# Kernel tuning notes

Hardware: AMD Instinct MI355X
Metric: run time of the kernel (lower is better)

Reference implementation:

```python
import jax, jax.numpy as jnp
import numpy as np

BS = 256          # batch size
N = 1000          # n_step_per_batch
ORDER = 2         # derivative order -> 3 vars (u, u', u'') per step
D = ORDER + 1
STEP_LOGIT = float(np.log(0.001 / 0.999))  # logit(0.001); sigmoid -> 0.001 step size


def mlp(x, w1, b1, w2, b2, w3, b3):
    h = jax.nn.relu(x @ w1 + b1)
    h = jax.nn.relu(h @ w2 + b2)
    return h @ w3 + b3


def build_A(c, h):
    # c: (N, 3) per-step equation coefficients; h: (N-1,) step sizes.
    # Rows: [1 initial-value] + [N equation] + [2*(N-1) Taylor smoothness (d=0,1)].
    R = 1 + N + 2 * (N - 1)
    i = jnp.arange(N)
    j = jnp.arange(N - 1)
    ones = jnp.ones(N - 1, c.dtype)
    rows = jnp.concatenate([
        jnp.array([0]),
        jnp.repeat(1 + i, 3),
        jnp.repeat(1 + N + 2 * j, 4),
        jnp.repeat(2 + N + 2 * j, 3)])
    cols = jnp.concatenate([
        jnp.array([0]),
        (i[:, None] * 3 + jnp.arange(3)).ravel(),
        jnp.stack([3 * j, 3 * j + 1, 3 * j + 2, 3 * (j + 1)], axis=1).ravel(),
        jnp.stack([3 * j + 1, 3 * j + 2, 3 * j + 4], axis=1).ravel()])
    vals = jnp.concatenate([
        jnp.ones(1, c.dtype),
        c.ravel(),
        jnp.stack([-ones, -h, -h * h / 2, ones], axis=1).ravel(),
        jnp.stack([-ones, -h, ones], axis=1).ravel()])
    return jnp.zeros((R, 3 * N), c.dtype).at[rows, cols].add(vals)


def ode_solve(coeffs, rhs, init_iv, steps):
    # coeffs (bs,1,N,3), rhs (bs,N,1), init_iv (bs,1), steps (bs,1,N-1)
    # coeffs/steps are batch-uniform in this model -> single shared system matrix.
    c = coeffs[0, 0]
    h = steps[0, 0]
    A = build_A(c, h)                       # (R, 3N)
    R = A.shape[0]
    b = jnp.zeros((R, BS), A.dtype)
    b = b.at[0].set(init_iv[:, 0]).at[1:1 + N].set(rhs[:, :, 0].T)
    AtA = A.T @ A + 1e-8 * jnp.eye(3 * N, dtype=A.dtype)
    u = jnp.linalg.solve(AtA, A.T @ b)      # (3N, BS) least-squares trajectory
    resid = A @ u - b
    eps = jnp.sqrt(jnp.sum(resid * resid, axis=0))  # (BS,) equation slack norm
    u = u.reshape(N, 3, BS)
    x0 = u[:, 0].T[:, :, None]              # (bs, N, 1)
    x1 = u[:, 1].T[:, :, None]
    x2 = u[:, 2].T[:, :, None]
    return x0, x1, x2, eps, steps


def reference(pin, ptime, pw1, pb1, pw2, pb2, pw3, pb3,
              tw1, tb1, tw2, tb2, tw3, tb3,
              nw1, nb1, nw2, nb2, nw3, nb3, net_iv):
    xi = mlp(pin, pw1, pb1, pw2, pb2, pw3, pb3).reshape(1, 3)
    ts = mlp(ptime, tw1, tb1, tw2, tb2, tw3, tb3).reshape(1, N)
    xi = jnp.tile(xi, (BS, 1))
    ts = jnp.tile(ts, (BS, 1))
    alpha = xi[:, 0:1][:, None, :]                 # (bs,1,1)
    beta = xi[:, 1:2][:, None, :]
    powr = jax.nn.sigmoid(xi[:, 2:3][:, None, :])
    ts = ts[:, None, :]                            # (bs,1,N)
    var = mlp(net_iv.reshape(BS, -1), nw1, nb1, nw2, nb2, nw3, nb3).reshape(BS, 1, N)
    rhs = jnp.abs(alpha * ts + beta * ts ** 2) ** powr * var ** 2 + ts
    rhs = jnp.transpose(rhs, (0, 2, 1))            # (bs, N, 1)
    coeffs = jnp.broadcast_to(jnp.array([0.0, 1.0, 0.0], net_iv.dtype), (BS, 1, N, 3))
    init_iv = var[:, :, 0]                         # (bs, 1)
    steps = jax.nn.sigmoid(jnp.full((BS, 1, N - 1), STEP_LOGIT, net_iv.dtype))
    x0, x1, x2, eps, steps = ode_solve(coeffs, rhs, init_iv, steps)
    x0 = jnp.transpose(x0, (0, 2, 1))              # (bs, 1, N)
    var = jnp.transpose(var, (0, 2, 1))            # (bs, N, 1)
    return (x0, steps, eps, var, ts[:, 0, :], alpha, beta, powr)


def setup_inputs() -> dict:
    key = jax.random.key(0)
    ks = jax.random.split(key, 24)
    f32 = jnp.float32

    def w(k, shape, scale=0.03):
        return (scale * jax.random.normal(k, shape)).astype(f32)

    inp = {
        "pin": w(ks[0], (1, 64), 1.0),
        "ptime": w(ks[1], (1, 64), 1.0),
        "pw1": w(ks[2], (64, 1024)), "pb1": jnp.zeros((1024,), f32),
        "pw2": w(ks[3], (1024, 1024)), "pb2": jnp.zeros((1024,), f32),
        "pw3": w(ks[4], (1024, 3)), "pb3": jnp.zeros((3,), f32),
        "tw1": w(ks[5], (64, 1024)), "tb1": jnp.zeros((1024,), f32),
        "tw2": w(ks[6], (1024, 1024)), "tb2": jnp.zeros((1024,), f32),
        "tw3": w(ks[7], (1024, N)), "tb3": jnp.zeros((N,), f32),
        "nw1": w(ks[8], (N, 1024)), "nb1": jnp.zeros((1024,), f32),
        "nw2": w(ks[9], (1024, 1024)), "nb2": jnp.zeros((1024,), f32),
        "nw3": w(ks[10], (1024, N)), "nb3": jnp.zeros((N,), f32),
        "net_iv": jax.random.normal(ks[11], (BS, N)).astype(f32),
    }
    return inp
```

## Files before the change

### kernel.cpp

```cpp
#include <hip/hip_runtime.h>
#include <math.h>

#define NN 1000
#define NIT 4
#define NKT 16

typedef _Float16 f16;
typedef _Float16 f16x8 __attribute__((ext_vector_type(8)));
typedef _Float16 f16x2 __attribute__((ext_vector_type(2)));
typedef float    f32x4 __attribute__((ext_vector_type(4)));

#define WS_H1P 0
#define WS_H1T 1024
#define WS_H2P 2048
#define WS_H2T 3072
#define WS_TS  4096
#define WS_XI  5120
#define WF_H1  802816
#define WF_H2  1064960
#define WF_BT2 2375680
#define WF_BT3 3424256

#define O_X0    0
#define O_STEP  256000
#define O_EPS   511744
#define O_VAR   512000
#define O_TS    768000
#define O_ALPHA 1024000
#define O_BETA  1024256
#define O_POWR  1024512

__device__ __forceinline__ void conv_bt_body(int idx, const float* __restrict__ W, int K0, int NW,
                                             f16* __restrict__ BT, float (*T)[32][33])
{
    const int tid = threadIdx.x;
    const int tx = tid & 31, ty = tid >> 5;
    const int kt = (idx & 31) * 32, ntile = (idx >> 5) * 32;
    #pragma unroll
    for (int i = 0; i < 4; ++i) {
        int k = kt + ty + i * 8, n = ntile + tx;
        (*T)[ty + i * 8][tx] = (k < K0 && n < NW) ? W[(size_t)k * NW + n] : 0.f;
    }
    __syncthreads();
    #pragma unroll
    for (int i = 0; i < 4; ++i) {
        int n = ntile + ty + i * 8, k = kt + tx;
        BT[(size_t)n * 1024 + k] = (f16)(*T)[tx][ty + i * 8];
    }
}

__device__ __forceinline__ void l1_body(int sub, const float* __restrict__ pin,
    const float* __restrict__ pw1, const float* __restrict__ pb1,
    const float* __restrict__ ptime, const float* __restrict__ tw1, const float* __restrict__ tb1,
    float* __restrict__ ws, float* sin_)
{
    const int tid = threadIdx.x;
    const bool tp = sub >= 4;
    const float* in = tp ? ptime : pin;
    const float* W  = tp ? tw1 : pw1;
    const float* B  = tp ? tb1 : pb1;
    float* outp = ws + (tp ? WS_H1T : WS_H1P);
    const int bxl = sub & 3;
    if (tid < 64) sin_[tid] = in[tid];
    __syncthreads();
    const int u = bxl * 256 + tid;
    float acc = B[u];
    #pragma unroll 16
    for (int k = 0; k < 64; ++k) acc += sin_[k] * W[k * 1024 + u];
    outp[u] = fmaxf(acc, 0.f);
}

__device__ __forceinline__ void l2_body(int lb, const float* __restrict__ pw2, const float* __restrict__ pb2,
    const float* __restrict__ tw2, const float* __restrict__ tb2, float* __restrict__ ws,
    float (*red)[16][17])
{
    const bool tp = lb >= 64;
    const float* h = ws + (tp ? WS_H1T : WS_H1P);
    const float* W = tp ? tw2 : pw2;
    const float* B = tp ? tb2 : pb2;
    float* outp = ws + (tp ? WS_H2T : WS_H2P);
    const int u0 = (lb & 63) * 16;
    const int tid = threadIdx.x, ul = tid & 15, kc = tid >> 4;
    const float* wp = W + u0 + ul;
    float acc = 0.f;
    const int kbase = kc * 64;
    #pragma unroll 8
    for (int k = 0; k < 64; ++k) acc += h[kbase + k] * wp[(size_t)(kbase + k) * 1024];
    (*red)[kc][ul] = acc; __syncthreads();
    for (int s = 8; s; s >>= 1) { if (kc < s) (*red)[kc][ul] += (*red)[kc + s][ul]; __syncthreads(); }
    if (tid < 16) outp[u0 + tid] = fmaxf((*red)[0][tid] + B[u0 + tid], 0.f);
}

__device__ __forceinline__ void l3_body(int lb, const float* __restrict__ pw3, const float* __restrict__ pb3,
    const float* __restrict__ tw3, const float* __restrict__ tb3,
    float* __restrict__ ws, float* __restrict__ out,
    float (*red)[16][17], float* redx)
{
    const int tid = threadIdx.x;
    if (lb == 64) {
        const float* h2p = ws + WS_H2P;
        float p[3] = {0.f, 0.f, 0.f};
        for (int k = tid; k < 1024; k += 256) {
            float h = h2p[k];
            p[0] += h * pw3[k * 3 + 0];
            p[1] += h * pw3[k * 3 + 1];
            p[2] += h * pw3[k * 3 + 2];
        }
        float xi[3];
        #pragma unroll
        for (int j = 0; j < 3; ++j) {
            redx[tid] = p[j]; __syncthreads();
            for (int s = 128; s > 0; s >>= 1) {
                if (tid < s) redx[tid] += redx[tid + s];
                __syncthreads();
            }
            xi[j] = redx[0] + pb3[j];
            __syncthreads();
        }
        float alpha = xi[0], beta = xi[1];
        float powr = 1.f / (1.f + expf(-xi[2]));
        if (tid == 0) { ws[WS_XI + 0] = alpha; ws[WS_XI + 1] = beta; ws[WS_XI + 2] = powr; }
        out[O_ALPHA + tid] = alpha;
        out[O_BETA  + tid] = beta;
        out[O_POWR  + tid] = powr;
    } else {
        const float* h = ws + WS_H2T;
        const int u0 = lb * 16;
        const int ul = tid & 15, kc = tid >> 4;
        const int u = u0 + ul;
        float acc = 0.f;
        const int kbase = kc * 64;
        if (u < NN) {
            #pragma unroll 8
            for (int k = 0; k < 64; ++k) acc += h[kbase + k] * tw3[(size_t)(kbase + k) * NN + u];
        }
        (*red)[kc][ul] = acc; __syncthreads();
        for (int s = 8; s; s >>= 1) { if (kc < s) (*red)[kc][ul] += (*red)[kc + s][ul]; __syncthreads(); }
        if (tid < 16 && u0 + tid < NN) ws[WS_TS + u0 + tid] = (*red)[0][tid] + tb3[u0 + tid];
    }
}

__device__ __forceinline__ void gemm_conv_body(int bx,
    const float* __restrict__ Af, int ldA, int K0,
    const float* __restrict__ W, int NW, const float* __restrict__ bias,
    f16* __restrict__ Cf16,
    f16 (*As)[32][72], f16 (*Bs)[32][72])
{
    const int tid = threadIdx.x;
    const int lane = tid & 63, wave = tid >> 6;
    const int wm = wave >> 1, wn = wave & 1;
    const int m0 = (bx >> 5) * 32, n0b = (bx & 31) * 32;

    const int sarow = tid >> 3, sac = (tid & 7) * 8;
    const int sbk = (tid >> 3) * 2, sbn = (tid & 7) * 4;
    const int bcol_ok = (n0b + sbn) < NW;

    f16x8 pa; float4 pb0, pb1;

    auto loadA = [&](int k0, f16x8& o) {
        float4 x = {0.f,0.f,0.f,0.f}, y = {0.f,0.f,0.f,0.f};
        if (k0 + sac < K0) {
            const float* p = Af + (size_t)(m0 + sarow) * ldA + k0 + sac;
            x = *(const float4*)p;
            y = *(const float4*)(p + 4);
        }
        f16x8 h = {(f16)x.x,(f16)x.y,(f16)x.z,(f16)x.w,
                   (f16)y.x,(f16)y.y,(f16)y.z,(f16)y.w};
        o = h;
    };
    auto loadB = [&](int k0, float4& b0, float4& b1) {
        b0 = {0.f,0.f,0.f,0.f}; b1 = {0.f,0.f,0.f,0.f};
        const int r0 = k0 + sbk;
        if (bcol_ok) {
            const float* p = W + (size_t)r0 * NW + n0b + sbn;
            if (r0 < K0)     b0 = *(const float4*)p;
            if (r0 + 1 < K0) b1 = *(const float4*)(p + NW);
        }
    };
    auto storeA = [&](int buf, const f16x8& v) {
        *(f16x8*)&As[buf][sarow][sac] = v;
    };
    auto storeB = [&](int buf, const float4& b0, const float4& b1) {
        f16x2 v0 = {(f16)b0.x, (f16)b1.x}; *(f16x2*)&Bs[buf][sbn + 0][sbk] = v0;
        f16x2 v1 = {(f16)b0.y, (f16)b1.y}; *(f16x2*)&Bs[buf][sbn + 1][sbk] = v1;
        f16x2 v2 = {(f16)b0.z, (f16)b1.z}; *(f16x2*)&Bs[buf][sbn + 2][sbk] = v2;
        f16x2 v3 = {(f16)b0.w, (f16)b1.w}; *(f16x2*)&Bs[buf][sbn + 3][sbk] = v3;
    };

    f32x4 acc = {0.f, 0.f, 0.f, 0.f};

    loadA(0, pa); loadB(0, pb0, pb1);
    storeA(0, pa); storeB(0, pb0, pb1);
    loadA(64, pa); loadB(64, pb0, pb1);
    __syncthreads();

    const int arow = wm * 16 + (lane & 15);
    const int brow = wn * 16 + (lane & 15);
    const int kf = (lane >> 4) * 8;

    #pragma unroll 2
    for (int t = 0; t < NKT; ++t) {
        const int cur = t & 1;
        f16x8 na; float4 nb0 = {}, nb1 = {};
        if (t + 2 < NKT) { loadA((t + 2) * 64, na); loadB((t + 2) * 64, nb0, nb1); }

        const f16x8 a0 = *(const f16x8*)&As[cur][arow][kf];
        const f16x8 b0 = *(const f16x8*)&Bs[cur][brow][kf];
        acc = __builtin_amdgcn_mfma_f32_16x16x32_f16(a0, b0, acc, 0, 0, 0);
        const f16x8 a1 = *(const f16x8*)&As[cur][arow][32 + kf];
        const f16x8 b1 = *(const f16x8*)&Bs[cur][brow][32 + kf];
        acc = __builtin_amdgcn_mfma_f32_16x16x32_f16(a1, b1, acc, 0, 0, 0);

        __syncthreads();
        if (t + 1 < NKT) {
            storeA(cur ^ 1, pa);
            storeB(cur ^ 1, pb0, pb1);
        }
        pa = na; pb0 = nb0; pb1 = nb1;
        __syncthreads();
    }

    const int col = n0b + wn * 16 + (lane & 15);
    const int row = m0 + wm * 16 + (lane >> 4) * 4;
    const float bs = (col < NW) ? bias[col] : 0.f;
    #pragma unroll
    for (int j = 0; j < 4; ++j) {
        float v = fmaxf(acc[j] + bs, 0.f);
        Cf16[(size_t)(row + j) * 1024 + col] = (f16)v;
    }
}

template<bool F16OUT>
__device__ __forceinline__ void gemm16_body(int bx, const f16* __restrict__ A, const f16* __restrict__ BT,
    const float* __restrict__ bias, int NW, f16* __restrict__ Cf16, float* __restrict__ Cf32, int ldc,
    f16 (*As)[32][72], f16 (*Bs)[32][72])
{
    const int tid = threadIdx.x;
    const int lane = tid & 63, wave = tid >> 6;
    const int wm = wave >> 1, wn = wave & 1;
    const int m0 = (bx >> 5) * 32, n0 = (bx & 31) * 32;
    const int srow = tid >> 3, sc = tid & 7;
    const float4* gA = (const float4*)(A  + (size_t)(m0 + srow) * 1024 + sc * 8);
    const float4* gB = (const float4*)(BT + (size_t)(n0 + srow) * 1024 + sc * 8);

    f32x4 acc = {0.f, 0.f, 0.f, 0.f};

    float4 ra = gA[0], rb = gB[0];
    *(float4*)&As[0][srow][sc * 8] = ra;
    *(float4*)&Bs[0][srow][sc * 8] = rb;
    ra = gA[8]; rb = gB[8];
    __syncthreads();

    const int arow = wm * 16 + (lane & 15);
    const int brow = wn * 16 + (lane & 15);
    const int kf = (lane >> 4) * 8;

    #pragma unroll 2
    for (int t = 0; t < NKT; ++t) {
        const int cur = t & 1;
        float4 ra2 = {}, rb2 = {};
        if (t + 2 < NKT) { ra2 = gA[(t + 2) * 8]; rb2 = gB[(t + 2) * 8]; }

        const f16x8 a0 = *(const f16x8*)&As[cur][arow][kf];
        const f16x8 b0 = *(const f16x8*)&Bs[cur][brow][kf];
        acc = __builtin_amdgcn_mfma_f32_16x16x32_f16(a0, b0, acc, 0, 0, 0);
        const f16x8 a1 = *(const f16x8*)&As[cur][arow][32 + kf];
        const f16x8 b1 = *(const f16x8*)&Bs[cur][brow][32 + kf];
        acc = __builtin_amdgcn_mfma_f32_16x16x32_f16(a1, b1, acc, 0, 0, 0);

        __syncthreads();
        if (t + 1 < NKT) {
            *(float4*)&As[cur ^ 1][srow][sc * 8] = ra;
            *(float4*)&Bs[cur ^ 1][srow][sc * 8] = rb;
        }
        ra = ra2; rb = rb2;
        __syncthreads();
    }

    const int col = n0 + wn * 16 + (lane & 15);
    const int row = m0 + wm * 16 + (lane >> 4) * 4;
    const float bs = (col < NW) ? bias[col] : 0.f;
    #pragma unroll
    for (int j = 0; j < 4; ++j) {
        float v = acc[j] + bs;
        if (F16OUT) {
            v = fmaxf(v, 0.f);
            Cf16[(size_t)(row + j) * 1024 + col] = (f16)v;
        } else if (col < NW) {
            Cf32[(size_t)(row + j) * ldc + col] = v;
        }
    }
}

__global__ __launch_bounds__(256) void k_s1(const float* __restrict__ net_iv,
    const float* __restrict__ nw1, const float* __restrict__ nb1, const float* __restrict__ nw2,
    const float* __restrict__ pin, const float* __restrict__ pw1, const float* __restrict__ pb1,
    const float* __restrict__ ptime, const float* __restrict__ tw1, const float* __restrict__ tb1,
    float* __restrict__ ws, f16* __restrict__ wsh)
{
    __shared__ f16 As[2][32][72];
    __shared__ f16 Bs[2][32][72];
    __shared__ float T[32][33];
    __shared__ float sin_[64];
    const int bx = blockIdx.x;
    if (bx < 256) {
        gemm_conv_body(bx, net_iv, 1000, 1000, nw1, 1024, nb1, wsh + WF_H1, As, Bs);
    } else if (bx < 264) {
        l1_body(bx - 256, pin, pw1, pb1, ptime, tw1, tb1, ws, sin_);
    } else {
        conv_bt_body(bx - 264, nw2, 1024, 1024, wsh + WF_BT2, &T);
    }
}

__global__ __launch_bounds__(256) void k_s2(const float* __restrict__ nw3, const float* __restrict__ nb2,
    const float* __restrict__ pw2, const float* __restrict__ pb2,
    const float* __restrict__ tw2, const float* __restrict__ tb2,
    float* __restrict__ ws, f16* __restrict__ wsh)
{
    __shared__ f16 As[2][32][72];
    __shared__ f16 Bs[2][32][72];
    __shared__ float T[32][33];
    __shared__ float red[16][17];
    const int bx = blockIdx.x;
    if (bx < 256) {
        gemm16_body<true>(bx, wsh + WF_H1, wsh + WF_BT2, nb2, 1024, wsh + WF_H2, nullptr, 0, As, Bs);
    } else if (bx < 1280) {
        conv_bt_body(bx - 256, nw3, 1024, 1000, wsh + WF_BT3, &T);
    } else {
        l2_body(bx - 1280, pw2, pb2, tw2, tb2, ws, &red);
    }
}

__global__ __launch_bounds__(256) void k_s3(const float* __restrict__ nb3,
    const float* __restrict__ pw3, const float* __restrict__ pb3,
    const float* __restrict__ tw3, const float* __restrict__ tb3,
    float* __restrict__ ws, f16* __restrict__ wsh, float* __restrict__ out)
{
    __shared__ f16 As[2][32][72];
    __shared__ f16 Bs[2][32][72];
    __shared__ float red[16][17];
    __shared__ float redx[256];
    const int bx = blockIdx.x;
    if (bx < 256) {
        gemm16_body<false>(bx, wsh + WF_H2, wsh + WF_BT3, nb3, 1000,
                           nullptr, out + O_VAR, 1000, As, Bs);
    } else {
        l3_body(bx - 256, pw3, pb3, tw3, tb3, ws, out, &red, redx);
    }
}

__device__ inline void d_shift_left(const double a[4], double b4[4], double* sh, int tid, double pad)
{
    __syncthreads();
    sh[tid] = a[0];
    __syncthreads();
    b4[0] = a[1]; b4[1] = a[2]; b4[2] = a[3];
    b4[3] = (tid < 255) ? sh[tid + 1] : pad;
}
__device__ inline void d_scan_fwd(const double a[4], double incl[4], double* swt, int tid)
{
    double p0 = a[0], p1 = p0 + a[1], p2 = p1 + a[2], p3 = p2 + a[3];
    int lane = tid & 63, wid = tid >> 6;
    double w = p3;
    #pragma unroll
    for (int d = 1; d < 64; d <<= 1) {
        double t = __shfl_up(w, d, 64);
        if (lane >= d) w += t;
    }
    __syncthreads();
    if (lane == 63) swt[wid] = w;
    __syncthreads();
    double off = w - p3;
    #pragma unroll
    for (int q = 0; q < 3; ++q) if (q < wid) off += swt[q];
    incl[0] = p0 + off; incl[1] = p1 + off; incl[2] = p2 + off; incl[3] = p3 + off;
}
__device__ inline void d_scan_rev(const double a[4], double incl[4], double* swt, int tid)
{
    double s3 = a[3], s2 = s3 + a[2], s1 = s2 + a[1], s0 = s1 + a[0];
    int lane = tid & 63, wid = tid >> 6;
    double w = s0;
    #pragma unroll
    for (int d = 1; d < 64; d <<= 1) {
        double t = __shfl_down(w, d, 64);
        if (lane < 64 - d) w += t;
    }
    __syncthreads();
    if (lane == 0) swt[wid] = w;
    __syncthreads();
    double off = w - s0;
    #pragma unroll
    for (int q = 1; q < 4; ++q) if (q > wid) off += swt[q];
    incl[0] = s0 + off; incl[1] = s1 + off; incl[2] = s2 + off; incl[3] = s3 + off;
}

__global__ __launch_bounds__(256) void k_ode(const float* __restrict__ ws, float* __restrict__ out)
{
    const int b = blockIdx.x;
    const int tid = threadIdx.x;
    const double H = 0.001, H2c = 0.5e-6, INVH = 1000.0, EPSR = 1e-8;

    __shared__ double sh[257];
    __shared__ double swt[4];

    const float alpha = ws[WS_XI + 0], beta = ws[WS_XI + 1], powr = ws[WS_XI + 2];

    const float4 tsv = *(const float4*)&ws[WS_TS + tid * 4];
    const float* varp = out + O_VAR + (size_t)b * NN;
    float vaa[4];
    #pragma unroll
    for (int k = 0; k < 4; ++k) {
        int i = tid * 4 + k;
        vaa[k] = (i < NN) ? varp[i] : 0.f;
    }
    const double init = (double)varp[0];

    float tsa[4] = {tsv.x, tsv.y, tsv.z, tsv.w};

    double r[4];
    #pragma unroll
    for (int k = 0; k < 4; ++k) {
        int i = tid * 4 + k;
        float tf = tsa[k], vf = vaa[k];
        float basef = fabsf(alpha * tf + beta * tf * tf);
        float rr = powf(basef, powr) * vf * vf + tf;
        r[k] = (i < NN) ? (double)rr : 0.0;
    }

    double rn[4];
    d_shift_left(r, rn, sh, tid, 0.0);
    double ux[4], ud[4], us[4], g[4], gi[4];
    #pragma unroll
    for (int k = 0; k < 4; ++k) {
        int i = tid * 4 + k;
        ud[k] = r[k];
        us[k] = (i < NN - 1) ? (rn[k] - r[k]) * INVH : 0.0;
        g[k]  = (i < NN - 1) ? 0.5 * H * (r[k] + rn[k]) : 0.0;
    }
    d_scan_fwd(g, gi, swt, tid);
    #pragma unroll
    for (int k = 0; k < 4; ++k) {
        int i = tid * 4 + k;
        ux[k] = (i < NN) ? (init + (gi[k] - g[k])) : 0.0;
    }

    double tx[4] = {0,0,0,0}, td[4] = {0,0,0,0}, tss[4] = {0,0,0,0};
    for (int it = 0; it < NIT; ++it) {
        double a[4], yx0 = 0.0;
        #pragma unroll
        for (int k = 0; k < 4; ++k) {
            int i = tid * 4 + k;
            double yx = ux[k] - EPSR * tx[k];
            if (k == 0) yx0 = yx;
            a[k] = (i == 0) ? 0.0 : yx;
        }
        double S[4]; d_scan_rev(a, S, swt, tid);
        double wP[4];
        #pragma unroll
        for (int k = 0; k < 4; ++k) wP[k] = S[k] - a[k];
        double wV[4];
        #pragma unroll
        for (int k = 0; k < 4; ++k) {
            int i = tid * 4 + k;
            double ys = us[k] - EPSR * tss[k];
            wV[k] = (i < NN - 1) ? -(ys + H2c * wP[k]) * INVH : 0.0;
        }
        __syncthreads();
        sh[tid] = wV[3];
        if (tid == 0) sh[256] = yx0 + wP[0];
        __syncthreads();
        double wVm[4];
        wVm[1] = wV[0]; wVm[2] = wV[1]; wVm[3] = wV[2];
        wVm[0] = (tid > 0) ? sh[tid - 1] : 0.0;
        const double w0 = sh[256];

        double wD[4];
        #pragma unroll
        for (int k = 0; k < 4; ++k) {
            int i = tid * 4 + k;
            double yd = ud[k] - EPSR * td[k];
            wD[k] = (i < NN) ? (yd + ((i < NN - 1) ? H * wP[k] : 0.0) - wVm[k] + wV[k]) : 0.0;
        }
        double wDn[4]; d_shift_left(wD, wDn, sh, tid, 0.0);
        #pragma unroll
        for (int k = 0; k < 4; ++k) {
            int i = tid * 4 + k;
            td[k]  = wD[k];
            tss[k] = (i < NN - 1) ? (wDn[k] - wD[k] - wV[k]) * INVH : 0.0;
            g[k]   = (i < NN - 1) ? (H * td[k] + H2c * tss[k] + wP[k]) : 0.0;
        }
        d_scan_fwd(g, gi, swt, tid);
        #pragma unroll
        for (int k = 0; k < 4; ++k) {
            int i = tid * 4 + k;
            tx[k] = (i < NN) ? (w0 + (gi[k] - g[k])) : 0.0;
        }
    }

    double dx[4], dd[4], ds_[4];
    #pragma unroll
    for (int k = 0; k < 4; ++k) { dx[k] = -EPSR * tx[k]; dd[k] = -EPSR * td[k]; ds_[k] = -EPSR * tss[k]; }

    #pragma unroll
    for (int k = 0; k < 4; ++k) {
        int i = tid * 4 + k;
        if (i < NN) {
            out[O_X0  + b * NN + i] = (float)(ux[k] + dx[k]);
            out[O_TS  + b * NN + i] = tsa[k];
        }
        if (i < NN - 1) out[O_STEP + b * (NN - 1) + i] = 0.001f;
    }

    double dxn[4], ddn[4];
    d_shift_left(dx, dxn, sh, tid, 0.0);
    d_shift_left(dd, ddn, sh, tid, 0.0);
    double ss = 0.0;
    #pragma unroll
    for (int k = 0; k < 4; ++k) {
        int i = tid * 4 + k;
        if (i < NN) ss += dd[k] * dd[k];
        if (i == 0) ss += dx[k] * dx[k];
        if (i < NN - 1) {
            double rp = dxn[k] - dx[k] - H * dd[k] - H2c * ds_[k];
            double rv = ddn[k] - dd[k] - H * ds_[k];
            ss += rp * rp + rv * rv;
        }
    }
    const int lane = tid & 63, wid = tid >> 6;
    #pragma unroll
    for (int d = 32; d; d >>= 1) ss += __shfl_down(ss, d, 64);
    __syncthreads();
    if (lane == 0) swt[wid] = ss;
    __syncthreads();
    if (tid == 0) out[O_EPS + b] = (float)sqrt(swt[0] + swt[1] + swt[2] + swt[3]);
}

extern "C" void kernel_launch(void* const* d_in, const int* in_sizes, int n_in,
                              void* d_out, int out_size, void* d_ws, size_t ws_size,
                              hipStream_t stream)
{
    const float* pin    = (const float*)d_in[0];
    const float* ptime  = (const float*)d_in[1];
    const float* pw1    = (const float*)d_in[2];
    const float* pb1    = (const float*)d_in[3];
    const float* pw2    = (const float*)d_in[4];
    const float* pb2    = (const float*)d_in[5];
    const float* pw3    = (const float*)d_in[6];
    const float* pb3    = (const float*)d_in[7];
    const float* tw1    = (const float*)d_in[8];
    const float* tb1    = (const float*)d_in[9];
    const float* tw2    = (const float*)d_in[10];
    const float* tb2    = (const float*)d_in[11];
    const float* tw3    = (const float*)d_in[12];
    const float* tb3    = (const float*)d_in[13];
    const float* nw1    = (const float*)d_in[14];
    const float* nb1    = (const float*)d_in[15];
    const float* nw2    = (const float*)d_in[16];
    const float* nb2    = (const float*)d_in[17];
    const float* nw3    = (const float*)d_in[18];
    const float* nb3    = (const float*)d_in[19];
    const float* net_iv = (const float*)d_in[20];
    float* out = (float*)d_out;
    float* ws  = (float*)d_ws;
    f16*   wsh = (f16*)d_ws;

    k_s1 <<<1288, 256, 0, stream>>>(net_iv, nw1, nb1, nw2, pin, pw1, pb1, ptime, tw1, tb1, ws, wsh);
    k_s2 <<<1408, 256, 0, stream>>>(nw3, nb2, pw2, pb2, tw2, tb2, ws, wsh);
    k_s3 <<<321,  256, 0, stream>>>(nb3, pw3, pb3, tw3, tb3, ws, wsh, out);
    k_ode<<<256,  256, 0, stream>>>(ws, out);
}
```

Before: 45.31 us.

## Replace LDS-staged GEMM with per-wave direct-load MFMA tiles and halve NIT

The 256x1024x1024 fp16 GEMMs in stages 2 and 3 no longer stage A and B tiles through shared memory with double buffering and barriers. Each wave now computes its own 16x16 output tile, loading MFMA operands directly from global memory and relying on cache for reuse. This removes the LDS traffic and the two block barriers per k-step, but adds redundant global or L2 reads across waves. NIT also drops from 4 to 2, cutting the iteration count of the later solver stage at some risk to numerical accuracy.

```diff
diff --git a/kernel.cpp b/kernel.cpp
--- a/kernel.cpp
+++ b/kernel.cpp
@@ -2,7 +2,7 @@
 #include <math.h>
 
 #define NN 1000
-#define NIT 4
+#define NIT 2
 #define NKT 16
 
 typedef _Float16 f16;
@@ -231,54 +231,29 @@
 }
 
 template<bool F16OUT>
-__device__ __forceinline__ void gemm16_body(int bx, const f16* __restrict__ A, const f16* __restrict__ BT,
-    const float* __restrict__ bias, int NW, f16* __restrict__ Cf16, float* __restrict__ Cf32, int ldc,
-    f16 (*As)[32][72], f16 (*Bs)[32][72])
+__device__ __forceinline__ void gemm16_nolds(int bx, const f16* __restrict__ A, const f16* __restrict__ BT,
+    const float* __restrict__ bias, int NW, f16* __restrict__ Cf16, float* __restrict__ Cf32, int ldc)
 {
     const int tid = threadIdx.x;
     const int lane = tid & 63, wave = tid >> 6;
-    const int wm = wave >> 1, wn = wave & 1;
-    const int m0 = (bx >> 5) * 32, n0 = (bx & 31) * 32;
-    const int srow = tid >> 3, sc = tid & 7;
-    const float4* gA = (const float4*)(A  + (size_t)(m0 + srow) * 1024 + sc * 8);
-    const float4* gB = (const float4*)(BT + (size_t)(n0 + srow) * 1024 + sc * 8);
+    const int t = bx * 4 + wave;
+    const int m0 = (t >> 6) * 16;
+    const int n0 = (t & 63) * 16;
+    const int kf = (lane >> 4) * 8;
+
+    const f16* pa = A  + (size_t)(m0 + (lane & 15)) * 1024 + kf;
+    const f16* pb = BT + (size_t)(n0 + (lane & 15)) * 1024 + kf;
 
     f32x4 acc = {0.f, 0.f, 0.f, 0.f};
-
-    float4 ra = gA[0], rb = gB[0];
-    *(float4*)&As[0][srow][sc * 8] = ra;
-    *(float4*)&Bs[0][srow][sc * 8] = rb;
-    ra = gA[8]; rb = gB[8];
-    __syncthreads();
-
-    const int arow = wm * 16 + (lane & 15);
-    const int brow = wn * 16 + (lane & 15);
-    const int kf = (lane >> 4) * 8;
-
-    #pragma unroll 2
-    for (int t = 0; t < NKT; ++t) {
-        const int cur = t & 1;
-        float4 ra2 = {}, rb2 = {};
-        if (t + 2 < NKT) { ra2 = gA[(t + 2) * 8]; rb2 = gB[(t + 2) * 8]; }
-
-        const f16x8 a0 = *(const f16x8*)&As[cur][arow][kf];
-        const f16x8 b0 = *(const f16x8*)&Bs[cur][brow][kf];
-        acc = __builtin_amdgcn_mfma_f32_16x16x32_f16(a0, b0, acc, 0, 0, 0);
-        const f16x8 a1 = *(const f16x8*)&As[cur][arow][32 + kf];
-        const f16x8 b1 = *(const f16x8*)&Bs[cur][brow][32 + kf];
-        acc = __builtin_amdgcn_mfma_f32_16x16x32_f16(a1, b1, acc, 0, 0, 0);
-
-        __syncthreads();
-        if (t + 1 < NKT) {
-            *(float4*)&As[cur ^ 1][srow][sc * 8] = ra;
-            *(float4*)&Bs[cur ^ 1][srow][sc * 8] = rb;
-        }
-        ra = ra2; rb = rb2;
-        __syncthreads();
-    }
-
-    const int col = n0 + wn * 16 + (lane & 15);
-    const int row = m0 + wm * 16 + (lane >> 4) * 4;
+    #pragma unroll 8
+    for (int k0 = 0; k0 < 1024; k0 += 32) {
+        const f16x8 a = *(const f16x8*)(pa + k0);
+        const f16x8 b = *(const f16x8*)(pb + k0);
+        acc = __builtin_amdgcn_mfma_f32_16x16x32_f16(a, b, acc, 0, 0, 0);
+    }
+
+    const int col = n0 + (lane & 15);
+    const int row = m0 + (lane >> 4) * 4;
     const float bs = (col < NW) ? bias[col] : 0.f;
     #pragma unroll
     for (int j = 0; j < 4; ++j) {
@@ -317,13 +292,11 @@
     const float* __restrict__ tw2, const float* __restrict__ tb2,
     float* __restrict__ ws, f16* __restrict__ wsh)
 {
-    __shared__ f16 As[2][32][72];
-    __shared__ f16 Bs[2][32][72];
     __shared__ float T[32][33];
     __shared__ float red[16][17];
     const int bx = blockIdx.x;
     if (bx < 256) {
-        gemm16_body<true>(bx, wsh + WF_H1, wsh + WF_BT2, nb2, 1024, wsh + WF_H2, nullptr, 0, As, Bs);
+        gemm16_nolds<true>(bx, wsh + WF_H1, wsh + WF_BT2, nb2, 1024, wsh + WF_H2, nullptr, 0);
     } else if (bx < 1280) {
         conv_bt_body(bx - 256, nw3, 1024, 1000, wsh + WF_BT3, &T);
     } else {
@@ -336,14 +309,12 @@
     const float* __restrict__ tw3, const float* __restrict__ tb3,
     float* __restrict__ ws, f16* __restrict__ wsh, float* __restrict__ out)
 {
-    __shared__ f16 As[2][32][72];
-    __shared__ f16 Bs[2][32][72];
     __shared__ float red[16][17];
     __shared__ float redx[256];
     const int bx = blockIdx.x;
     if (bx < 256) {
-        gemm16_body<false>(bx, wsh + WF_H2, wsh + WF_BT3, nb3, 1000,
-                           nullptr, out + O_VAR, 1000, As, Bs);
+        gemm16_nolds<false>(bx, wsh + WF_H2, wsh + WF_BT3, nb3, 1000,
+                            nullptr, out + O_VAR, 1000);
     } else {
         l3_body(bx - 256, pw3, pb3, tw3, tb3, ws, out, &red, redx);
     }
```

After: 49.55 us. +9.4%, slower.
